# Kernel optimization log

Measured on AMD Instinct MI355X. Metric: run time of the kernel, lower is better.

Reference implementation:

```python
import jax, jax.numpy as jnp
import numpy as np
import math

NUM_SECTORS = 8
HIDDEN = 128
FEAT = 64
MAX_DIST = 10.0


def gru_last(x, Wih, Whh, bih, bhh):
    # PyTorch GRU (gate order r,z,n); x: (B,T,D) -> last hidden (B,H)
    B = x.shape[0]
    H = Whh.shape[1]
    xp = jnp.einsum('btd,gd->btg', x, Wih) + bih  # (B,T,3H)

    def step(h, xpt):
        hp = h @ Whh.T + bhh
        xr, xz, xn = jnp.split(xpt, 3, -1)
        hr, hz, hn = jnp.split(hp, 3, -1)
        r = jax.nn.sigmoid(xr + hr)
        z = jax.nn.sigmoid(xz + hz)
        n = jnp.tanh(xn + r * hn)
        h_new = (1.0 - z) * n + z * h
        return h_new, None

    h0 = jnp.zeros((B, H), x.dtype)
    hT, _ = jax.lax.scan(step, h0, jnp.swapaxes(xp, 0, 1))
    return hT


def setup_inputs() -> dict:
    key = jax.random.key(0)
    ks = iter(jax.random.split(key, 32))
    B, N, T = 2048, 64, 8
    H, Hn = HIDDEN, HIDDEN // 2
    s = 0.05

    def p(shape):
        return jax.random.normal(next(ks), shape, jnp.float32) * s

    inp = {
        'target_trajectory': jax.random.normal(next(ks), (B, T, 2), jnp.float32),
        'neighbor_trajectories': jax.random.normal(next(ks), (B, N, T, 2), jnp.float32),
        'relative_angles': jax.random.uniform(next(ks), (B, N), jnp.float32) * (2.0 * math.pi),
        'neighbor_mask': (jax.random.uniform(next(ks), (B, N)) > 0.2).astype(jnp.float32),
        # target GRU (H=128)
        'Wih_t': p((3 * H, 2)), 'Whh_t': p((3 * H, H)), 'bih_t': p((3 * H,)), 'bhh_t': p((3 * H,)),
        # neighbor GRU (H=64)
        'Wih_n': p((3 * Hn, 2)), 'Whh_n': p((3 * Hn, Hn)), 'bih_n': p((3 * Hn,)), 'bhh_n': p((3 * Hn,)),
        # sector encoder: 68 -> 128 -> 128
        'W1': p((H, 4 + Hn)), 'b1': p((H,)), 'W2': p((H, H)), 'b2': p((H,)),
        # fusion: 1152 -> 256 -> 128 -> 64
        'Wf1': p((2 * H, H + NUM_SECTORS * H)), 'bf1': p((2 * H,)),
        'Wf2': p((H, 2 * H)), 'bf2': p((H,)),
        'Wf3': p((FEAT, H)), 'bf3': p((FEAT,)),
        'ln_g': jnp.ones((FEAT,), jnp.float32), 'ln_b': jnp.zeros((FEAT,), jnp.float32),
    }
    return inp


def reference(target_trajectory, neighbor_trajectories, relative_angles, neighbor_mask,
              Wih_t, Whh_t, bih_t, bhh_t, Wih_n, Whh_n, bih_n, bhh_n,
              W1, b1, W2, b2, Wf1, bf1, Wf2, bf2, Wf3, bf3, ln_g, ln_b):
    B, N, T, D = neighbor_trajectories.shape
    S = NUM_SECTORS

    # trajectory encoders
    target_feature = gru_last(target_trajectory, Wih_t, Whh_t, bih_t, bhh_t)  # (B,128)
    nf = gru_last(neighbor_trajectories.reshape(B * N, T, D), Wih_n, Whh_n, bih_n, bhh_n)
    nf = nf.reshape(B, N, -1)  # (B,N,64)

    # geometry
    target_pos = target_trajectory[:, -1, :]                      # (B,2)
    npos = neighbor_trajectories[:, :, -1, :]                     # (B,N,2)
    dist = jnp.linalg.norm(npos - target_pos[:, None, :], axis=-1)  # (B,N)
    vel = neighbor_trajectories[:, :, -1, :] - neighbor_trajectories[:, :, -2, :]  # (B,N,2)

    # sector assignment (vectorized segment reduce over sectors)
    sector_size = 2.0 * math.pi / S
    sid = jnp.clip((relative_angles / sector_size).astype(jnp.int32), 0, S - 1)  # (B,N)
    valid = neighbor_mask > 0
    memb = ((sid[..., None] == jnp.arange(S)) & valid[..., None]).astype(dist.dtype)  # (B,N,S)

    count = memb.sum(1)                        # (B,S)
    nonempty = count > 0
    safe = jnp.maximum(count, 1.0)
    avg_d = jnp.where(nonempty, (dist[..., None] * memb).sum(1) / safe, 0.0)  # (B,S)
    avg_v = jnp.where(nonempty[..., None], jnp.einsum('bns,bnc->bsc', memb, vel) / safe[..., None], 0.0)

    w = jnp.exp(-dist / MAX_DIST)              # (B,N)
    wm = w[..., None] * memb                   # (B,N,S)
    wsum = wm.sum(1) + 1e-8                    # (B,S)
    wfeat = jnp.einsum('bns,bnh->bsh', wm, nf) / wsum[..., None]  # (B,S,64)

    sector_feats = jnp.concatenate([count[..., None], avg_d[..., None], avg_v, wfeat], axis=-1)  # (B,S,68)

    # sector encoder MLP (dropout off / eval)
    h = jax.nn.relu(sector_feats @ W1.T + b1)
    h = jax.nn.relu(h @ W2.T + b2)             # (B,S,128)
    enc = h.reshape(B, S * HIDDEN)

    combined = jnp.concatenate([target_feature, enc], axis=-1)  # (B,1152)
    f = jax.nn.relu(combined @ Wf1.T + bf1)
    f = jax.nn.relu(f @ Wf2.T + bf2)
    f = jax.nn.relu(f @ Wf3.T + bf3)           # (B,64)

    mu = f.mean(-1, keepdims=True)
    var = ((f - mu) ** 2).mean(-1, keepdims=True)
    return (f - mu) / jnp.sqrt(var + 1e-5) * ln_g + ln_b
```

## Files before the change

### kernel.cpp

```cpp
#include <hip/hip_runtime.h>

typedef __attribute__((ext_vector_type(8))) short short8;
typedef __attribute__((ext_vector_type(4))) float f32x4;

#define SGC (-1.44269504088896341f)
#define THC ( 2.88539008177792681f)

__device__ __forceinline__ unsigned short f2bf(float f){
  unsigned u = __float_as_uint(f);
  return (unsigned short)((u + 0x7fffu + ((u >> 16) & 1u)) >> 16);
}
__device__ __forceinline__ float bf2f(unsigned short b){
  return __uint_as_float(((unsigned)b) << 16);
}
__device__ __forceinline__ unsigned f2bf_cvt(float f){
  unsigned r;
  asm("v_cvt_pk_bf16_f32 %0, %1, %1" : "=v"(r) : "v"(f));
  return r;
}
__device__ __forceinline__ unsigned f2bf_pk(float lo, float hi){
  unsigned r;
  asm("v_cvt_pk_bf16_f32 %0, %1, %2" : "=v"(r) : "v"(lo), "v"(hi));
  return r;
}

__global__ __launch_bounds__(256) void k_prep(
    const float* __restrict__ Whh_t, const float* __restrict__ W1,
    const float* __restrict__ W2,    const float* __restrict__ Wf1,
    const float* __restrict__ Wf2,   const float* __restrict__ Wf3,
    const float* __restrict__ Whh_n,
    unsigned short* __restrict__ wgt)
{
  int i = blockIdx.x * 256 + threadIdx.x;
  if (i < 49152){
    int g = i >> 7;
    float s = (g < 256) ? SGC : THC;
    wgt[i] = f2bf(Whh_t[i] * s); return;
  }
  i -= 49152;
  if (i < 12288){ int r = i / 96, c = i % 96;
    wgt[49152 + i] = (c < 68) ? f2bf(W1[r*68 + c]) : (unsigned short)0; return; }
  i -= 12288;
  if (i < 16384){ wgt[61440 + i] = f2bf(W2[i]); return; }
  i -= 16384;
  if (i < 294912){ wgt[77824 + i] = f2bf(Wf1[i]); return; }
  i -= 294912;
  if (i < 32768){ wgt[372736 + i] = f2bf(Wf2[i]); return; }
  i -= 32768;
  if (i < 8192){ wgt[405504 + i] = f2bf(Wf3[i]); return; }
  i -= 8192;
  if (i < 12288){
    int g = i >> 6;
    float s = (g < 128) ? SGC : THC;
    wgt[413696 + i] = f2bf(Whh_n[i] * s); return;
  }
}

__global__ __launch_bounds__(512, 4) void k_gru_n(
    const float* __restrict__ ttraj, const float* __restrict__ ntraj,
    const float* __restrict__ rang,  const float* __restrict__ nmask,
    const float* __restrict__ Wih_n,
    const float* __restrict__ bih_n, const float* __restrict__ bhh_n,
    const unsigned short* __restrict__ wgt,
    unsigned short* __restrict__ sf)
{
  __shared__ char smem[54272];
  const int tid = threadIdx.x;
  const int bi = tid >> 8, lt = tid & 255;
  const int w = lt >> 6, u = (lt >> 4) & 3, c = lt & 15;
  const int b = blockIdx.x * 2 + bi;
  const unsigned short* whhN_b = wgt + 413696;

  unsigned short* whh2 = (unsigned short*)smem;
  unsigned short* wx   = whh2 + 12288;
  char* pb = smem + 27648 + bi * 13312;
  unsigned short* hall = (unsigned short*)pb;
  unsigned short* hb   = hall + w * 1152;
  float* xst  = (float*)(pb + 9216);

  for (int i = tid; i < 1536; i += 512){
    int nt = i >> 7, rem = i & 127;
    int hf = rem >> 6, uu = (rem >> 4) & 3, cc = rem & 15;
    *(short8*)&whh2[nt*1024 + hf*512 + (uu*16+cc)*8] =
        *(const short8*)&whhN_b[(nt*16+cc)*64 + hf*32 + uu*8];
  }
  if (tid < 192){
    int t = tid >> 4, cc = tid & 15;
    float s = (t < 8) ? SGC : THC;
    int g = (t < 4) ? (t*16 + cc) : (t < 8) ? (64 + (t-4)*16 + cc) : (128 + (t-8)*16 + cc);
    float bsum = (t < 8) ? (bih_n[g] + bhh_n[g]) : bih_n[g];
    unsigned short* p = &wx[t*128 + cc*8];
    *(short8*)p = (short8){0,0,0,0,0,0,0,0};
    p[0] = f2bf(Wih_n[g*2]   * s);
    p[1] = f2bf(Wih_n[g*2+1] * s);
    p[2] = f2bf(bsum * s);
  }
  {
    float4 v = ((const float4*)(ntraj + (size_t)b * 1024))[lt];
    int seq = lt >> 2, s0 = (lt & 3) * 2;
    xst[s0*128 + seq*2]       = v.x;
    xst[s0*128 + seq*2 + 1]   = v.y;
    xst[(s0+1)*128 + seq*2]   = v.z;
    xst[(s0+1)*128 + seq*2+1] = v.w;
  }
  __syncthreads();

  float bh_[4];
#pragma unroll
  for (int gt = 0; gt < 4; ++gt) bh_[gt] = bhh_n[128 + gt*16 + c] * THC;

  float hcur[4][4];
#pragma unroll
  for (int gt=0; gt<4; ++gt)
#pragma unroll
    for (int q=0; q<4; ++q) hcur[gt][q] = 0.0f;

  auto gates = [&](int gt, const f32x4& aR, const f32x4& aZ, const f32x4& aN, const f32x4& aX){
#pragma unroll
    for (int q = 0; q < 4; ++q){
      float r = __builtin_amdgcn_rcpf(1.0f + __builtin_amdgcn_exp2f(aR[q]));
      float z = __builtin_amdgcn_rcpf(1.0f + __builtin_amdgcn_exp2f(aZ[q]));
      float hn = aN[q] + bh_[gt];
      float pn = __builtin_fmaf(r, hn, aX[q]);
      float E = __builtin_amdgcn_exp2f(pn);
      float n = __builtin_fmaf(-2.0f, __builtin_amdgcn_rcpf(E + 1.0f), 1.0f);
      float hnew = __builtin_fmaf(z, hcur[gt][q] - n, n);
      hcur[gt][q] = hnew;
      hb[(u*4+q)*72 + gt*16 + c] = (unsigned short)f2bf_cvt(hnew);
    }
  };

  const int lane8 = (u*16 + c) * 8;
  const f32x4 zz = {0.f,0.f,0.f,0.f};

  for (int st = 0; st < 8; ++st){
    float2 xv = *(const float2*)&xst[st*128 + (w*16+c)*2];
    unsigned p01 = f2bf_pk(xv.x, xv.y);
    bool u0 = (u == 0);
    union { unsigned ui[4]; short8 s8; } a2u;
    a2u.ui[0] = u0 ? p01 : 0u;
    a2u.ui[1] = u0 ? 0x3F80u : 0u;
    a2u.ui[2] = 0u; a2u.ui[3] = 0u;
    short8 a2 = a2u.s8;

    if (st > 0){
      short8 a0 = *(short8*)&hb[c*72 + u*8];
      short8 a1 = *(short8*)&hb[c*72 + 32 + u*8];
#pragma unroll
      for (int gt = 0; gt < 4; ++gt){
        const unsigned short* pr = whh2 + gt*1024 + lane8;
        const unsigned short* pz = whh2 + (4+gt)*1024 + lane8;
        const unsigned short* pq = whh2 + (8+gt)*1024 + lane8;
        short8 bxr = *(const short8*)&wx[gt*128 + c*8];
        short8 bxz = *(const short8*)&wx[(4+gt)*128 + c*8];
        short8 bxn = *(const short8*)&wx[(8+gt)*128 + c*8];
        f32x4 aR = __builtin_amdgcn_mfma_f32_16x16x32_bf16(a0, *(const short8*)pr, zz, 0,0,0);
        aR = __builtin_amdgcn_mfma_f32_16x16x32_bf16(a1, *(const short8*)(pr+512), aR, 0,0,0);
        aR = __builtin_amdgcn_mfma_f32_16x16x32_bf16(a2, bxr, aR, 0,0,0);
        f32x4 aZ = __builtin_amdgcn_mfma_f32_16x16x32_bf16(a0, *(const short8*)pz, zz, 0,0,0);
        aZ = __builtin_amdgcn_mfma_f32_16x16x32_bf16(a1, *(const short8*)(pz+512), aZ, 0,0,0);
        aZ = __builtin_amdgcn_mfma_f32_16x16x32_bf16(a2, bxz, aZ, 0,0,0);
        f32x4 aN = __builtin_amdgcn_mfma_f32_16x16x32_bf16(a0, *(const short8*)pq, zz, 0,0,0);
        aN = __builtin_amdgcn_mfma_f32_16x16x32_bf16(a1, *(const short8*)(pq+512), aN, 0,0,0);
        f32x4 aX = __builtin_amdgcn_mfma_f32_16x16x32_bf16(a2, bxn, zz, 0,0,0);
        gates(gt, aR, aZ, aN, aX);
      }
    } else {
#pragma unroll
      for (int gt = 0; gt < 4; ++gt){
        short8 bxr = *(const short8*)&wx[gt*128 + c*8];
        short8 bxz = *(const short8*)&wx[(4+gt)*128 + c*8];
        short8 bxn = *(const short8*)&wx[(8+gt)*128 + c*8];
        f32x4 aR = __builtin_amdgcn_mfma_f32_16x16x32_bf16(a2, bxr, zz, 0,0,0);
        f32x4 aZ = __builtin_amdgcn_mfma_f32_16x16x32_bf16(a2, bxz, zz, 0,0,0);
        f32x4 aX = __builtin_amdgcn_mfma_f32_16x16x32_bf16(a2, bxn, zz, 0,0,0);
        gates(gt, aR, aZ, zz, aX);
      }
    }
  }
  __syncthreads();

  if (lt < 64){
    int n = lt;
    float m   = nmask[(size_t)b*64 + n];
    float ang = rang[(size_t)b*64 + n];
    float tx = ttraj[(size_t)b*16 + 14], ty = ttraj[(size_t)b*16 + 15];
    float px = xst[7*128 + n*2], py = xst[7*128 + n*2 + 1];
    float vx = px - xst[6*128 + n*2], vy = py - xst[6*128 + n*2 + 1];
    float dx = px - tx, dy = py - ty;
    float dist = __builtin_amdgcn_sqrtf(dx*dx + dy*dy);
    int sid = (int)(ang / 0.78539816339744830962f);
    sid = sid < 0 ? 0 : (sid > 7 ? 7 : sid);
    bool valid = m > 0.0f;
    float wv = valid ? __builtin_amdgcn_exp2f(dist * -0.14426950408889634f) : 0.0f;
    xst[n]       = valid ? dist : 0.0f;
    xst[64 + n]  = valid ? vx   : 0.0f;
    xst[128 + n] = valid ? vy   : 0.0f;
    xst[192 + n] = wv;
    xst[256 + n] = valid ? (float)sid : -1.0f;
  }
  __syncthreads();
  if (lt < 8){
    int s = lt;
    float cnt=0.f, sd=0.f, sx=0.f, sy=0.f, sw=0.f;
    for (int n=0; n<64; ++n){
      if (xst[256+n] == (float)s){
        cnt += 1.f; sd += xst[n]; sx += xst[64+n]; sy += xst[128+n]; sw += xst[192+n];
      }
    }
    float inv = (cnt > 0.f) ? __builtin_amdgcn_rcpf(cnt) : 0.f;
    xst[320 + s] = cnt;
    xst[328 + s] = sd * inv;
    xst[336 + s] = sx * inv;
    xst[344 + s] = sy * inv;
    xst[352 + s] = __builtin_amdgcn_rcpf(sw + 1e-8f);
  }
  __syncthreads();
#pragma unroll
  for (int rep = 0; rep < 2; ++rep){
    int p = lt + rep*256;
    int s = p >> 6, h = p & 63;
    float fs = (float)s;
    float a = 0.f;
    for (int n = 0; n < 64; ++n){
      float wmv = (xst[256+n] == fs) ? xst[192+n] : 0.f;
      float nf  = bf2f(hall[(n>>4)*1152 + (n&15)*72 + h]);
      a += wmv * nf;
    }
    sf[((size_t)b*8 + s)*96 + 4 + h] = (unsigned short)f2bf_cvt(a * xst[352+s]);
  }
  if (lt < 32){
    int s = lt >> 2, cc = lt & 3;
    sf[((size_t)b*8 + s)*96 + cc] = (unsigned short)f2bf_cvt(xst[320 + cc*8 + s]);
  }
  if (lt < 224){
    int s = lt / 28, cc = 68 + lt % 28;
    sf[((size_t)b*8 + s)*96 + cc] = 0;
  }
}

__global__ __launch_bounds__(256) void k_gru_t(
    const float* __restrict__ ttraj,
    const float* __restrict__ Wih_t, const float* __restrict__ bih_t, const float* __restrict__ bhh_t,
    const unsigned short* __restrict__ wgt,
    unsigned short* __restrict__ combined)
{
  __shared__ char smem[9728];
  const int tid = threadIdx.x, w = tid >> 6, u = (tid >> 4) & 3, c = tid & 15;
  unsigned short* hb0 = (unsigned short*)smem;
  unsigned short* hb1 = (unsigned short*)(smem + 4352);
  float* xs = (float*)(smem + 8704);

  xs[tid] = ttraj[(size_t)blockIdx.x*256 + tid];

  int ntg[6];
  ntg[0] = 2*w; ntg[1] = 2*w+1;
  ntg[2] = 8+2*w; ntg[3] = 9+2*w;
  ntg[4] = 16+2*w; ntg[5] = 17+2*w;

  short8 Bf[6][4];
#pragma unroll
  for (int lt2 = 0; lt2 < 6; ++lt2){
    const unsigned short* wp = wgt + (ntg[lt2]*16 + c)*128 + u*8;
#pragma unroll
    for (int kk = 0; kk < 4; ++kk)
      Bf[lt2][kk] = *(const short8*)(wp + kk*32);
  }

  float Wr0[2],Wr1[2],BR[2],Wz0[2],Wz1[2],BZ[2],Wn0[2],Wn1[2],BI[2],BH[2];
#pragma unroll
  for (int gt = 0; gt < 2; ++gt){
    int g = w*32 + gt*16 + c;
    Wr0[gt]=Wih_t[g*2]*SGC;        Wr1[gt]=Wih_t[g*2+1]*SGC;        BR[gt]=(bih_t[g]+bhh_t[g])*SGC;
    Wz0[gt]=Wih_t[(128+g)*2]*SGC;  Wz1[gt]=Wih_t[(128+g)*2+1]*SGC;  BZ[gt]=(bih_t[128+g]+bhh_t[128+g])*SGC;
    Wn0[gt]=Wih_t[(256+g)*2]*THC;  Wn1[gt]=Wih_t[(256+g)*2+1]*THC;  BI[gt]=bih_t[256+g]*THC; BH[gt]=bhh_t[256+g]*THC;
  }
  float hcur[2][4];
#pragma unroll
  for (int gt=0; gt<2; ++gt)
#pragma unroll
    for (int q=0; q<4; ++q) hcur[gt][q] = 0.0f;
  __syncthreads();

  for (int st = 0; st < 8; ++st){
    unsigned short* rbuf = (st & 1) ? hb0 : hb1;
    unsigned short* wbuf = (st & 1) ? hb1 : hb0;
    f32x4 acc[6];
    if (st > 0){
      short8 a0 = *(short8*)&rbuf[c*136 + u*8];
      short8 a1 = *(short8*)&rbuf[c*136 + 32 + u*8];
      short8 a2 = *(short8*)&rbuf[c*136 + 64 + u*8];
      short8 a3 = *(short8*)&rbuf[c*136 + 96 + u*8];
#pragma unroll
      for (int lt2 = 0; lt2 < 6; ++lt2){
        f32x4 t = {0.f,0.f,0.f,0.f};
        t = __builtin_amdgcn_mfma_f32_16x16x32_bf16(a0, Bf[lt2][0], t, 0,0,0);
        t = __builtin_amdgcn_mfma_f32_16x16x32_bf16(a1, Bf[lt2][1], t, 0,0,0);
        t = __builtin_amdgcn_mfma_f32_16x16x32_bf16(a2, Bf[lt2][2], t, 0,0,0);
        acc[lt2] = __builtin_amdgcn_mfma_f32_16x16x32_bf16(a3, Bf[lt2][3], t, 0,0,0);
      }
    } else {
#pragma unroll
      for (int lt2 = 0; lt2 < 6; ++lt2) acc[lt2] = (f32x4){0.f,0.f,0.f,0.f};
    }
#pragma unroll
    for (int gt = 0; gt < 2; ++gt){
#pragma unroll
      for (int q = 0; q < 4; ++q){
        int sq = u*4 + q;
        float x0 = xs[sq*16 + st*2], x1 = xs[sq*16 + st*2 + 1];
        float rp = __builtin_fmaf(Wr0[gt], x0, __builtin_fmaf(Wr1[gt], x1, acc[gt][q] + BR[gt]));
        float zp = __builtin_fmaf(Wz0[gt], x0, __builtin_fmaf(Wz1[gt], x1, acc[2+gt][q] + BZ[gt]));
        float r = __builtin_amdgcn_rcpf(1.0f + __builtin_amdgcn_exp2f(rp));
        float z = __builtin_amdgcn_rcpf(1.0f + __builtin_amdgcn_exp2f(zp));
        float hnv = acc[4+gt][q] + BH[gt];
        float pn = __builtin_fmaf(Wn0[gt], x0, __builtin_fmaf(Wn1[gt], x1, __builtin_fmaf(r, hnv, BI[gt])));
        float E = __builtin_amdgcn_exp2f(pn);
        float n = __builtin_fmaf(-2.0f, __builtin_amdgcn_rcpf(E + 1.0f), 1.0f);
        float hnew = __builtin_fmaf(z, hcur[gt][q] - n, n);
        hcur[gt][q] = hnew;
        if (st < 7){
          wbuf[sq*136 + w*32 + gt*16 + c] = (unsigned short)f2bf_cvt(hnew);
        } else {
          int row = blockIdx.x*16 + sq;
          combined[(size_t)row*1152 + w*32 + gt*16 + c] = (unsigned short)f2bf_cvt(hnew);
        }
      }
    }
    if (st < 7) __syncthreads();
  }
}

__global__ __launch_bounds__(256) void k_mlp12(
    const unsigned short* __restrict__ sf,
    const unsigned short* __restrict__ wgt,
    const float* __restrict__ b1, const float* __restrict__ b2,
    unsigned short* __restrict__ combined)
{
  __shared__ char smem[18432];
  unsigned short* hb = (unsigned short*)smem + (threadIdx.x >> 6) * 2176;
  float* b1s = (float*)(smem + 17408);
  float* b2s = b1s + 128;
  const unsigned short* w1b = wgt + 49152;
  const unsigned short* w2b = wgt + 61440;
  const int tid = threadIdx.x, w = tid >> 6, u = (tid >> 4) & 3, c = tid & 15;
  if (tid < 128){ b1s[tid] = b1[tid]; b2s[tid] = b2[tid]; }
  __syncthreads();
  const int rowb = blockIdx.x * 64 + w * 16;

  f32x4 acc[8];
#pragma unroll
  for (int nt=0; nt<8; ++nt) acc[nt] = (f32x4){0.f,0.f,0.f,0.f};
#pragma unroll
  for (int kc=0; kc<3; ++kc){
    short8 a = *(const short8*)&sf[(size_t)(rowb + c)*96 + kc*32 + u*8];
#pragma unroll
    for (int nt=0; nt<8; ++nt){
      short8 bb = *(const short8*)&w1b[(nt*16+c)*96 + kc*32 + u*8];
      acc[nt] = __builtin_amdgcn_mfma_f32_16x16x32_bf16(a, bb, acc[nt], 0,0,0);
    }
  }
#pragma unroll
  for (int nt=0; nt<8; ++nt){
    float bias = b1s[nt*16+c];
#pragma unroll
    for (int q=0; q<4; ++q){
      float v = acc[nt][q] + bias; v = v > 0.f ? v : 0.f;
      hb[(u*4+q)*136 + nt*16 + c] = (unsigned short)f2bf_cvt(v);
    }
  }
  f32x4 acc2[8];
#pragma unroll
  for (int nt=0; nt<8; ++nt) acc2[nt] = (f32x4){0.f,0.f,0.f,0.f};
#pragma unroll
  for (int kc=0; kc<4; ++kc){
    short8 a = *(short8*)&hb[c*136 + kc*32 + u*8];
#pragma unroll
    for (int nt=0; nt<8; ++nt){
      short8 bb = *(const short8*)&w2b[(nt*16+c)*128 + kc*32 + u*8];
      acc2[nt] = __builtin_amdgcn_mfma_f32_16x16x32_bf16(a, bb, acc2[nt], 0,0,0);
    }
  }
#pragma unroll
  for (int nt=0; nt<8; ++nt){
    float bias = b2s[nt*16+c];
#pragma unroll
    for (int q=0; q<4; ++q){
      float v = acc2[nt][q] + bias; v = v > 0.f ? v : 0.f;
      int r = rowb + u*4 + q;
      combined[(size_t)(r >> 3)*1152 + 128 + (r & 7)*128 + nt*16 + c] = (unsigned short)f2bf_cvt(v);
    }
  }
}

__global__ __launch_bounds__(256) void k_head(
    const unsigned short* __restrict__ combined,
    const unsigned short* __restrict__ wgt,
    const float* __restrict__ bf1, const float* __restrict__ bf2, const float* __restrict__ bf3,
    const float* __restrict__ lng, const float* __restrict__ lnb,
    float* __restrict__ out)
{
  __shared__ char smem[15104];
  const int tid = threadIdx.x, w = tid >> 6, u = (tid >> 4) & 3, c = tid & 15;
  unsigned short* f1b = (unsigned short*)smem;
  unsigned short* f2b = (unsigned short*)(smem + 8448);
  float* bf1s = (float*)(smem + 12800); float* bf2s = (float*)(smem + 13824);
  float* bf3s = (float*)(smem + 14336);
  float* lngs = (float*)(smem + 14592); float* lnbs = (float*)(smem + 14848);
  const unsigned short* wf1b = wgt + 77824;
  const unsigned short* wf2b = wgt + 372736;
  const unsigned short* wf3b = wgt + 405504;
  bf1s[tid] = bf1[tid];
  if (tid < 128) bf2s[tid] = bf2[tid];
  if (tid < 64){ bf3s[tid] = bf3[tid]; lngs[tid] = lng[tid]; lnbs[tid] = lnb[tid]; }
  __syncthreads();
  const int rowb = blockIdx.x * 16;

  f32x4 acc[4];
#pragma unroll
  for (int i=0; i<4; ++i) acc[i] = (f32x4){0.f,0.f,0.f,0.f};
#pragma unroll 4
  for (int kc=0; kc<36; ++kc){
    short8 a = *(const short8*)&combined[(size_t)(rowb + c)*1152 + kc*32 + u*8];
#pragma unroll
    for (int i=0; i<4; ++i){
      int nt = w*4 + i;
      short8 bb = *(const short8*)&wf1b[(size_t)(nt*16+c)*1152 + kc*32 + u*8];
      acc[i] = __builtin_amdgcn_mfma_f32_16x16x32_bf16(a, bb, acc[i], 0,0,0);
    }
  }
#pragma unroll
  for (int i=0; i<4; ++i){
    int nt = w*4 + i;
    float bias = bf1s[nt*16+c];
#pragma unroll
    for (int q=0; q<4; ++q){
      float v = acc[i][q] + bias; v = v > 0.f ? v : 0.f;
      f1b[(u*4+q)*264 + nt*16 + c] = (unsigned short)f2bf_cvt(v);
    }
  }
  __syncthreads();

  f32x4 acc2[2];
#pragma unroll
  for (int i=0; i<2; ++i) acc2[i] = (f32x4){0.f,0.f,0.f,0.f};
#pragma unroll
  for (int kc=0; kc<8; ++kc){
    short8 a = *(short8*)&f1b[c*264 + kc*32 + u*8];
#pragma unroll
    for (int i=0; i<2; ++i){
      int nt = w*2 + i;
      short8 bb = *(const short8*)&wf2b[(nt*16+c)*256 + kc*32 + u*8];
      acc2[i] = __builtin_amdgcn_mfma_f32_16x16x32_bf16(a, bb, acc2[i], 0,0,0);
    }
  }
#pragma unroll
  for (int i=0; i<2; ++i){
    int nt = w*2 + i;
    float bias = bf2s[nt*16+c];
#pragma unroll
    for (int q=0; q<4; ++q){
      float v = acc2[i][q] + bias; v = v > 0.f ? v : 0.f;
      f2b[(u*4+q)*136 + nt*16 + c] = (unsigned short)f2bf_cvt(v);
    }
  }
  __syncthreads();

  f32x4 acc3[4];
#pragma unroll
  for (int nt=0; nt<4; ++nt) acc3[nt] = (f32x4){0.f,0.f,0.f,0.f};
#pragma unroll
  for (int kc=0; kc<4; ++kc){
    short8 a = *(short8*)&f2b[c*136 + kc*32 + u*8];
#pragma unroll
    for (int nt=0; nt<4; ++nt){
      short8 bb = *(const short8*)&wf3b[(nt*16+c)*128 + kc*32 + u*8];
      acc3[nt] = __builtin_amdgcn_mfma_f32_16x16x32_bf16(a, bb, acc3[nt], 0,0,0);
    }
  }
  if (w == 0){
    float v[4][4];
#pragma unroll
    for (int nt=0; nt<4; ++nt){
      float bias = bf3s[nt*16+c];
#pragma unroll
      for (int q=0; q<4; ++q){
        float t = acc3[nt][q] + bias; v[nt][q] = t > 0.f ? t : 0.f;
      }
    }
#pragma unroll
    for (int q=0; q<4; ++q){
      float p = v[0][q] + v[1][q] + v[2][q] + v[3][q];
      p += __shfl_xor(p, 1); p += __shfl_xor(p, 2); p += __shfl_xor(p, 4); p += __shfl_xor(p, 8);
      float mu = p * 0.015625f;
      float d0 = v[0][q]-mu, d1 = v[1][q]-mu, d2 = v[2][q]-mu, d3 = v[3][q]-mu;
      float p2 = d0*d0 + d1*d1 + d2*d2 + d3*d3;
      p2 += __shfl_xor(p2, 1); p2 += __shfl_xor(p2, 2); p2 += __shfl_xor(p2, 4); p2 += __shfl_xor(p2, 8);
      float rstd = __builtin_amdgcn_rsqf(p2 * 0.015625f + 1e-5f);
      int row = rowb + u*4 + q;
#pragma unroll
      for (int nt=0; nt<4; ++nt){
        int col = nt*16 + c;
        out[(size_t)row*64 + col] = (v[nt][q] - mu) * rstd * lngs[col] + lnbs[col];
      }
    }
  }
}

extern "C" void kernel_launch(void* const* d_in, const int* in_sizes, int n_in,
                              void* d_out, int out_size, void* d_ws, size_t ws_size,
                              hipStream_t stream)
{
  const float* ttraj = (const float*)d_in[0];
  const float* ntraj = (const float*)d_in[1];
  const float* rang  = (const float*)d_in[2];
  const float* nmask = (const float*)d_in[3];
  const float* Wih_t = (const float*)d_in[4];
  const float* Whh_t = (const float*)d_in[5];
  const float* bih_t = (const float*)d_in[6];
  const float* bhh_t = (const float*)d_in[7];
  const float* Wih_n = (const float*)d_in[8];
  const float* Whh_n = (const float*)d_in[9];
  const float* bih_n = (const float*)d_in[10];
  const float* bhh_n = (const float*)d_in[11];
  const float* W1  = (const float*)d_in[12];
  const float* b1  = (const float*)d_in[13];
  const float* W2  = (const float*)d_in[14];
  const float* b2  = (const float*)d_in[15];
  const float* Wf1 = (const float*)d_in[16];
  const float* bf1 = (const float*)d_in[17];
  const float* Wf2 = (const float*)d_in[18];
  const float* bf2 = (const float*)d_in[19];
  const float* Wf3 = (const float*)d_in[20];
  const float* bf3 = (const float*)d_in[21];
  const float* lng = (const float*)d_in[22];
  const float* lnb = (const float*)d_in[23];

  char* ws = (char*)d_ws;
  unsigned short* combined = (unsigned short*)ws;
  unsigned short* sf       = (unsigned short*)(ws + 5242880);
  unsigned short* wgt      = (unsigned short*)(ws + 8388608);

  hipLaunchKernelGGL(k_prep, dim3(1664), dim3(256), 0, stream,
                     Whh_t, W1, W2, Wf1, Wf2, Wf3, Whh_n, wgt);
  hipLaunchKernelGGL(k_gru_n, dim3(1024), dim3(512), 0, stream,
                     ttraj, ntraj, rang, nmask, Wih_n, bih_n, bhh_n, wgt, sf);
  hipLaunchKernelGGL(k_gru_t, dim3(128), dim3(256), 0, stream,
                     ttraj, Wih_t, bih_t, bhh_t, wgt, combined);
  hipLaunchKernelGGL(k_mlp12, dim3(256), dim3(256), 0, stream, sf, wgt, b1, b2, combined);
  hipLaunchKernelGGL(k_head, dim3(128), dim3(256), 0, stream,
                     combined, wgt, bf1, bf2, bf3, lng, lnb, (float*)d_out);
}
```

Baseline: 135.2 us.

## Run neighbor GRU one batch per block, pack inputs to bf16, hoist Wx fragments

The neighbor-GRU kernel now handles one batch element per 256-thread block instead of two per 512-thread block, doubling the grid and shrinking LDS per block. Trajectory inputs are pre-packed to bf16 pairs in shared memory, and the input-weight MFMA fragments are loaded into registers once instead of every step. Post-GRU pooling reads last positions from global memory. The aim is better occupancy and scheduling flexibility plus fewer LDS reads in the recurrent loop, at the cost of restaging the recurrent weights into LDS twice as many times and holding more registers.

```diff
diff --git a/kernel.cpp b/kernel.cpp
--- a/kernel.cpp
+++ b/kernel.cpp
@@ -56,7 +56,7 @@
   }
 }
 
-__global__ __launch_bounds__(512, 4) void k_gru_n(
+__global__ __launch_bounds__(256, 4) void k_gru_n(
     const float* __restrict__ ttraj, const float* __restrict__ ntraj,
     const float* __restrict__ rang,  const float* __restrict__ nmask,
     const float* __restrict__ Wih_n,
@@ -64,21 +64,20 @@
     const unsigned short* __restrict__ wgt,
     unsigned short* __restrict__ sf)
 {
-  __shared__ char smem[54272];
+  __shared__ char smem[38912];
   const int tid = threadIdx.x;
-  const int bi = tid >> 8, lt = tid & 255;
-  const int w = lt >> 6, u = (lt >> 4) & 3, c = lt & 15;
-  const int b = blockIdx.x * 2 + bi;
+  const int w = tid >> 6, u = (tid >> 4) & 3, c = tid & 15;
+  const int b = blockIdx.x;
   const unsigned short* whhN_b = wgt + 413696;
 
   unsigned short* whh2 = (unsigned short*)smem;
   unsigned short* wx   = whh2 + 12288;
-  char* pb = smem + 27648 + bi * 13312;
-  unsigned short* hall = (unsigned short*)pb;
+  unsigned short* hall = (unsigned short*)(smem + 27648);
   unsigned short* hb   = hall + w * 1152;
-  float* xst  = (float*)(pb + 9216);
-
-  for (int i = tid; i < 1536; i += 512){
+  unsigned* xpk = (unsigned*)(smem + 36864);
+  float* pool   = (float*)(smem + 36864);
+
+  for (int i = tid; i < 1536; i += 256){
     int nt = i >> 7, rem = i & 127;
     int hf = rem >> 6, uu = (rem >> 4) & 3, cc = rem & 15;
     *(short8*)&whh2[nt*1024 + hf*512 + (uu*16+cc)*8] =
@@ -96,14 +95,16 @@
     p[2] = f2bf(bsum * s);
   }
   {
-    float4 v = ((const float4*)(ntraj + (size_t)b * 1024))[lt];
-    int seq = lt >> 2, s0 = (lt & 3) * 2;
-    xst[s0*128 + seq*2]       = v.x;
-    xst[s0*128 + seq*2 + 1]   = v.y;
-    xst[(s0+1)*128 + seq*2]   = v.z;
-    xst[(s0+1)*128 + seq*2+1] = v.w;
-  }
-  __syncthreads();
+    float4 v = ((const float4*)(ntraj + (size_t)b * 1024))[tid];
+    int n = tid >> 2, p = (tid & 3) * 2;
+    xpk[p*64 + n]       = f2bf_pk(v.x, v.y);
+    xpk[(p+1)*64 + n]   = f2bf_pk(v.z, v.w);
+  }
+  __syncthreads();
+
+  short8 BX[12];
+#pragma unroll
+  for (int t = 0; t < 12; ++t) BX[t] = *(const short8*)&wx[t*128 + c*8];
 
   float bh_[4];
 #pragma unroll
@@ -134,8 +135,7 @@
   const f32x4 zz = {0.f,0.f,0.f,0.f};
 
   for (int st = 0; st < 8; ++st){
-    float2 xv = *(const float2*)&xst[st*128 + (w*16+c)*2];
-    unsigned p01 = f2bf_pk(xv.x, xv.y);
+    unsigned p01 = xpk[st*64 + w*16 + c];
     bool u0 = (u == 0);
     union { unsigned ui[4]; short8 s8; } a2u;
     a2u.ui[0] = u0 ? p01 : 0u;
@@ -151,90 +151,85 @@
         const unsigned short* pr = whh2 + gt*1024 + lane8;
         const unsigned short* pz = whh2 + (4+gt)*1024 + lane8;
         const unsigned short* pq = whh2 + (8+gt)*1024 + lane8;
-        short8 bxr = *(const short8*)&wx[gt*128 + c*8];
-        short8 bxz = *(const short8*)&wx[(4+gt)*128 + c*8];
-        short8 bxn = *(const short8*)&wx[(8+gt)*128 + c*8];
         f32x4 aR = __builtin_amdgcn_mfma_f32_16x16x32_bf16(a0, *(const short8*)pr, zz, 0,0,0);
         aR = __builtin_amdgcn_mfma_f32_16x16x32_bf16(a1, *(const short8*)(pr+512), aR, 0,0,0);
-        aR = __builtin_amdgcn_mfma_f32_16x16x32_bf16(a2, bxr, aR, 0,0,0);
+        aR = __builtin_amdgcn_mfma_f32_16x16x32_bf16(a2, BX[gt], aR, 0,0,0);
         f32x4 aZ = __builtin_amdgcn_mfma_f32_16x16x32_bf16(a0, *(const short8*)pz, zz, 0,0,0);
         aZ = __builtin_amdgcn_mfma_f32_16x16x32_bf16(a1, *(const short8*)(pz+512), aZ, 0,0,0);
-        aZ = __builtin_amdgcn_mfma_f32_16x16x32_bf16(a2, bxz, aZ, 0,0,0);
+        aZ = __builtin_amdgcn_mfma_f32_16x16x32_bf16(a2, BX[4+gt], aZ, 0,0,0);
         f32x4 aN = __builtin_amdgcn_mfma_f32_16x16x32_bf16(a0, *(const short8*)pq, zz, 0,0,0);
         aN = __builtin_amdgcn_mfma_f32_16x16x32_bf16(a1, *(const short8*)(pq+512), aN, 0,0,0);
-        f32x4 aX = __builtin_amdgcn_mfma_f32_16x16x32_bf16(a2, bxn, zz, 0,0,0);
+        f32x4 aX = __builtin_amdgcn_mfma_f32_16x16x32_bf16(a2, BX[8+gt], zz, 0,0,0);
         gates(gt, aR, aZ, aN, aX);
       }
     } else {
 #pragma unroll
       for (int gt = 0; gt < 4; ++gt){
-        short8 bxr = *(const short8*)&wx[gt*128 + c*8];
-        short8 bxz = *(const short8*)&wx[(4+gt)*128 + c*8];
-        short8 bxn = *(const short8*)&wx[(8+gt)*128 + c*8];
-        f32x4 aR = __builtin_amdgcn_mfma_f32_16x16x32_bf16(a2, bxr, zz, 0,0,0);
-        f32x4 aZ = __builtin_amdgcn_mfma_f32_16x16x32_bf16(a2, bxz, zz, 0,0,0);
-        f32x4 aX = __builtin_amdgcn_mfma_f32_16x16x32_bf16(a2, bxn, zz, 0,0,0);
+        f32x4 aR = __builtin_amdgcn_mfma_f32_16x16x32_bf16(a2, BX[gt], zz, 0,0,0);
+        f32x4 aZ = __builtin_amdgcn_mfma_f32_16x16x32_bf16(a2, BX[4+gt], zz, 0,0,0);
+        f32x4 aX = __builtin_amdgcn_mfma_f32_16x16x32_bf16(a2, BX[8+gt], zz, 0,0,0);
         gates(gt, aR, aZ, zz, aX);
       }
     }
   }
   __syncthreads();
 
-  if (lt < 64){
-    int n = lt;
+  if (tid < 64){
+    int n = tid;
+    const float* nb = ntraj + (size_t)b*1024 + n*16;
+    float px = nb[14], py = nb[15];
+    float vx = px - nb[12], vy = py - nb[13];
     float m   = nmask[(size_t)b*64 + n];
     float ang = rang[(size_t)b*64 + n];
     float tx = ttraj[(size_t)b*16 + 14], ty = ttraj[(size_t)b*16 + 15];
-    float px = xst[7*128 + n*2], py = xst[7*128 + n*2 + 1];
-    float vx = px - xst[6*128 + n*2], vy = py - xst[6*128 + n*2 + 1];
     float dx = px - tx, dy = py - ty;
     float dist = __builtin_amdgcn_sqrtf(dx*dx + dy*dy);
     int sid = (int)(ang / 0.78539816339744830962f);
     sid = sid < 0 ? 0 : (sid > 7 ? 7 : sid);
     bool valid = m > 0.0f;
     float wv = valid ? __builtin_amdgcn_exp2f(dist * -0.14426950408889634f) : 0.0f;
-    xst[n]       = valid ? dist : 0.0f;
-    xst[64 + n]  = valid ? vx   : 0.0f;
-    xst[128 + n] = valid ? vy   : 0.0f;
-    xst[192 + n] = wv;
-    xst[256 + n] = valid ? (float)sid : -1.0f;
-  }
-  __syncthreads();
-  if (lt < 8){
-    int s = lt;
+    pool[n]       = valid ? dist : 0.0f;
+    pool[64 + n]  = valid ? vx   : 0.0f;
+    pool[128 + n] = valid ? vy   : 0.0f;
+    pool[192 + n] = wv;
+    pool[256 + n] = valid ? (float)sid : -1.0f;
+  }
+  __syncthreads();
+  if (tid < 8){
+    int s = tid;
     float cnt=0.f, sd=0.f, sx=0.f, sy=0.f, sw=0.f;
     for (int n=0; n<64; ++n){
-      if (xst[256+n] == (float)s){
-        cnt += 1.f; sd += xst[n]; sx += xst[64+n]; sy += xst[128+n]; sw += xst[192+n];
+      if (pool[256+n] == (float)s){
+        cnt += 1.f; sd += pool[n]; sx += pool[64+n]; sy += pool[128+n]; sw += pool[192+n];
       }
     }
     float inv = (cnt > 0.f) ? __builtin_amdgcn_rcpf(cnt) : 0.f;
-    xst[320 + s] = cnt;
-    xst[328 + s] = sd * inv;
-    xst[336 + s] = sx * inv;
-    xst[344 + s] = sy * inv;
-    xst[352 + s] = __builtin_amdgcn_rcpf(sw + 1e-8f);
+    pool[320 + s] = cnt;
+    pool[328 + s] = sd * inv;
+    pool[336 + s] = sx * inv;
+    pool[344 + s] = sy * inv;
+    pool[352 + s] = __builtin_amdgcn_rcpf(sw + 1e-8f);
   }
   __syncthreads();
 #pragma unroll
   for (int rep = 0; rep < 2; ++rep){
-    int p = lt + rep*256;
+    int p = tid + rep*256;
     int s = p >> 6, h = p & 63;
     float fs = (float)s;
     float a = 0.f;
     for (int n = 0; n < 64; ++n){
-      float wmv = (xst[256+n] == fs) ? xst[192+n] : 0.f;
+      float wmv = (pool[256+n] == fs) ? pool[192+n] : 0.f;
       float nf  = bf2f(hall[(n>>4)*1152 + (n&15)*72 + h]);
       a += wmv * nf;
     }
-    sf[((size_t)b*8 + s)*96 + 4 + h] = (unsigned short)f2bf_cvt(a * xst[352+s]);
-  }
-  if (lt < 32){
-    int s = lt >> 2, cc = lt & 3;
-    sf[((size_t)b*8 + s)*96 + cc] = (unsigned short)f2bf_cvt(xst[320 + cc*8 + s]);
-  }
-  if (lt < 224){
-    int s = lt / 28, cc = 68 + lt % 28;
+    sf[((size_t)b*8 + s)*96 + 4 + h] = (unsigned short)f2bf_cvt(a * pool[352+s]);
+  }
+  if (tid < 32){
+    int s = tid >> 2, cc = tid & 3;
+    sf[((size_t)b*8 + s)*96 + cc] = (unsigned short)f2bf_cvt(pool[320 + cc*8 + s]);
+  }
+  if (tid < 224){
+    int s = tid / 28, cc = 68 + tid % 28;
     sf[((size_t)b*8 + s)*96 + cc] = 0;
   }
 }
@@ -543,7 +538,7 @@
 
   hipLaunchKernelGGL(k_prep, dim3(1664), dim3(256), 0, stream,
                      Whh_t, W1, W2, Wf1, Wf2, Wf3, Whh_n, wgt);
-  hipLaunchKernelGGL(k_gru_n, dim3(1024), dim3(512), 0, stream,
+  hipLaunchKernelGGL(k_gru_n, dim3(2048), dim3(256), 0, stream,
                      ttraj, ntraj, rang, nmask, Wih_n, bih_n, bhh_n, wgt, sf);
   hipLaunchKernelGGL(k_gru_t, dim3(128), dim3(256), 0, stream,
                      ttraj, Wih_t, bih_t, bhh_t, wgt, combined);
```

Measured after the change: 135.1 us. No clear change (-0.1%).
